# Performance work log

Hardware: AMD Instinct MI355X
Metric: run time of the kernel (lower is better)

The kernel has to match this reference:

```python
import jax, jax.numpy as jnp
import numpy as np

N_NODES = 512
HEADS = 4
CO = 64        # per-head out channels (PyG GATConv out_channels)
NEG_SLOPE = 0.2  # PyG GATConv default negative_slope


def setup_inputs() -> dict:
    key = jax.random.key(0)
    k0, k1, k2, k3, k4 = jax.random.split(key, 5)
    B, C, T, N = 8, 64, 12, N_NODES
    E = 8192
    x = jax.random.normal(k0, (B, C, T, N), dtype=jnp.float32)
    edge_index = jax.random.randint(k1, (2, E), 0, N, dtype=jnp.int32)
    # learned params of GATConv(in=64, out=64, heads=4, concat=False)
    W = jax.random.normal(k2, (C, HEADS * CO), dtype=jnp.float32) / np.sqrt(C).astype(np.float32)
    att_src = jax.random.normal(k3, (HEADS, CO), dtype=jnp.float32) * 0.1
    att_dst = jax.random.normal(k4, (HEADS, CO), dtype=jnp.float32) * 0.1
    bias = jnp.zeros((CO,), dtype=jnp.float32)
    return {"x": x, "edge_index": edge_index, "W": W,
            "att_src": att_src, "att_dst": att_dst, "bias": bias}


def reference(x, edge_index, W, att_src, att_dst, bias):
    # x: [B, C, T, N] -> batch of G = B*T graphs, all sharing edge_index.
    B, C, T, N = x.shape
    H, Co = att_src.shape
    G = B * T
    xg = x.transpose(0, 2, 3, 1).reshape(G, N, C)              # [G,N,C]
    h = (xg @ W).reshape(G, N, H, Co)                          # [G,N,H,Co]
    a_src = jnp.einsum('gnhc,hc->gnh', h, att_src)             # [G,N,H]
    a_dst = jnp.einsum('gnhc,hc->gnh', h, att_dst)             # [G,N,H]
    # add self loops (PyG GATConv default)
    loops = jnp.arange(N, dtype=edge_index.dtype)
    src = jnp.concatenate([edge_index[0], loops])              # [E']
    dst = jnp.concatenate([edge_index[1], loops])              # [E']
    # attention logits per edge, leading edge axis for segment ops
    logits = jax.nn.leaky_relu(a_src[:, src] + a_dst[:, dst], NEG_SLOPE)  # [G,E',H]
    logits = logits.transpose(1, 0, 2)                         # [E',G,H]
    m = jax.ops.segment_max(logits, dst, num_segments=N)       # [N,G,H]
    e = jnp.exp(logits - m[dst])
    s = jax.ops.segment_sum(e, dst, num_segments=N)            # [N,G,H]
    alpha = e / s[dst]                                         # [E',G,H]  (dropout off: eval)
    msg = alpha[..., None] * h[:, src].transpose(1, 0, 2, 3)   # [E',G,H,Co]
    out = jax.ops.segment_sum(msg, dst, num_segments=N)        # [N,G,H,Co]
    out = out.mean(axis=2) + bias                              # [N,G,Co]  concat=False -> head mean
    out = out.transpose(1, 0, 2).reshape(B, T, N, Co)          # [B,T,N,Co]
    return out.transpose(0, 3, 1, 2)                           # [B,Co,T,N]
```

## Files before the change

### kernel.cpp

```cpp
#include <hip/hip_runtime.h>

#define B_  8
#define C_  64
#define T_  12
#define N_  512
#define E_  8192
#define H_  4
#define CO_ 64
#define G_  (B_ * T_)
#define EP_ (E_ + N_)
#define MAXDEG 128
#define POISON 0xAAAAAAAAu

typedef __bf16 bf16x8 __attribute__((ext_vector_type(8)));
typedef unsigned short usx8 __attribute__((ext_vector_type(8)));
typedef float  f32x4  __attribute__((ext_vector_type(4)));

static __device__ __forceinline__ unsigned short f2bf(float f) {
    unsigned int u = __float_as_uint(f);
    return (unsigned short)((u + 0x7fffu + ((u >> 16) & 1u)) >> 16);
}

__global__ __launch_bounds__(256) void k_prep(
    const float* __restrict__ x, const int* __restrict__ ei,
    const float* __restrict__ W,
    const float* __restrict__ att_src, const float* __restrict__ att_dst,
    unsigned short* __restrict__ xtb, float* __restrict__ as_, float* __restrict__ ad_,
    unsigned int* __restrict__ cnt, int* __restrict__ srclist,
    unsigned short* __restrict__ Wfrag)
{
    int bid = blockIdx.x, tid = threadIdx.x;

    if (bid >= 768) {
        if (bid < 800) {
            int e = (bid - 768) * 256 + tid;
            int d = ei[E_ + e], s = ei[e];
            unsigned int pos = atomicAdd(&cnt[d], 1u) - POISON;
            srclist[d * MAXDEG + pos] = s;
        } else {
            int base = (bid - 800) * 2048;
            #pragma unroll
            for (int it = 0; it < 8; ++it) {
                int idx = base + it * 256 + tid;
                int c  = idx >> 8, r = idx & 255;
                int hh = r >> 6,  co = r & 63;
                int k  = hh * 64 + c;
                int ks = k >> 5, kq = (k >> 3) & 3, j = k & 7;
                int nt = co >> 4, l = kq * 16 + (co & 15);
                Wfrag[(size_t)((ks * 4 + nt) * 64 + l) * 8 + j] = f2bf(W[idx]);
            }
        }
        return;
    }

    __shared__ float xs[64][65];
    __shared__ float Wls[64][4], Wld[64][4];
    __shared__ float sa[64][5], sd[64][5];

    int lane = tid & 63, q = tid >> 6;

    {
        float s1 = 0.f, s2 = 0.f;
        const float4* w4 = reinterpret_cast<const float4*>(W + lane * 256 + q * 64);
        const float4* a1 = reinterpret_cast<const float4*>(att_src + q * 64);
        const float4* a2 = reinterpret_cast<const float4*>(att_dst + q * 64);
        #pragma unroll
        for (int j = 0; j < 16; ++j) {
            float4 w = w4[j], u = a1[j], v = a2[j];
            s1 += w.x * u.x + w.y * u.y + w.z * u.z + w.w * u.w;
            s2 += w.x * v.x + w.y * v.y + w.z * v.z + w.w * v.w;
        }
        Wls[lane][q] = s1;
        Wld[lane][q] = s2;
    }

    int g  = bid >> 3, tl = bid & 7;
    int b  = g / T_, t = g - b * T_;
    int n0 = tl * 64;

    #pragma unroll
    for (int i = 0; i < 16; ++i) {
        int c = q + i * 4;
        xs[c][lane] = x[((size_t)(b * C_ + c) * T_ + t) * N_ + n0 + lane];
    }
    __syncthreads();

    float s1 = 0.f, s2 = 0.f;
    for (int c = 0; c < 64; ++c) {
        float v = xs[c][lane];
        s1 += v * Wls[c][q];
        s2 += v * Wld[c][q];
    }
    sa[lane][q] = s1;
    sd[lane][q] = s2;

    #pragma unroll
    for (int i = 0; i < 16; ++i) {
        int nl = q + i * 4;
        xtb[((size_t)(g * N_ + n0 + nl)) * 64 + lane] = f2bf(xs[lane][nl]);
    }
    __syncthreads();

    int nl = tid >> 2, hh = tid & 3;
    as_[((size_t)(g * N_ + n0 + nl)) * 4 + hh] = sa[nl][hh];
    ad_[((size_t)(g * N_ + n0 + nl)) * 4 + hh] = sd[nl][hh];
}

__global__ __launch_bounds__(256) void k_aggr(
    const unsigned short* __restrict__ xtb, const float* __restrict__ as_,
    const float* __restrict__ ad_,
    const unsigned int* __restrict__ cnt, const int* __restrict__ srclist,
    unsigned short* __restrict__ zb)
{
    __shared__ float wbuf[2][MAXDEG][4][4];
    __shared__ int   ssrc[2][MAXDEG];
    int tid  = threadIdx.x;
    int wave = tid >> 6, lane = tid & 63;
    int xcd  = blockIdx.x & 7;
    int slot = blockIdx.x >> 3;
    int np   = slot & 255;
    int gq   = slot >> 8;
    int g0   = xcd * 12 + gq * 4;
    int n0   = np * 2;
    int dg[2] = {(int)(cnt[n0] - POISON), (int)(cnt[n0 + 1] - POISON)};
    int dtot  = max(dg[0], dg[1]) + 1;

    {
        int row = tid >> 7, t2 = tid & 127;
        ssrc[row][t2] = (t2 < dg[row]) ? srclist[(n0 + row) * MAXDEG + t2]
                                       : (n0 + row);
    }

    int sub = tid & 15, p = tid >> 4;
    int hh = sub & 3, gl = sub >> 2;
    int gg = g0 + gl;
    #pragma unroll
    for (int u = 0; u < 2; ++u) {
        float adv = ad_[((size_t)(gg * N_ + n0 + u)) * 4 + hh];
        for (int e = p; e < dg[u]; e += 16) {
            int s = srclist[(n0 + u) * MAXDEG + e];
            float v = as_[((size_t)(gg * N_ + s)) * 4 + hh] + adv;
            v = v > 0.f ? v : 0.2f * v;
            wbuf[u][e][gl][hh] = __expf(v);
        }
        if (p == 0) {
            float v = as_[((size_t)(gg * N_ + n0 + u)) * 4 + hh] + adv;
            v = v > 0.f ? v : 0.2f * v;
            wbuf[u][dg[u]][gl][hh] = __expf(v);
        }
        for (int e = dg[u] + 1 + p; e < dtot; e += 16)
            wbuf[u][e][gl][hh] = 0.f;
    }
    __syncthreads();

    int g   = g0 + wave;
    int u   = lane >> 5;
    int ch2 = (lane & 31) * 2;
    const unsigned short* xg = xtb + ((size_t)g * N_) * 64 + ch2;

    float zA0 = 0.f, zA1 = 0.f, zA2 = 0.f, zA3 = 0.f;
    float zB0 = 0.f, zB1 = 0.f, zB2 = 0.f, zB3 = 0.f;
    float s0 = 0.f, s1 = 0.f, s2 = 0.f, s3 = 0.f;
    int e = 0;
    for (; e + 8 <= dtot; e += 8) {
        unsigned int xv[8];
        #pragma unroll
        for (int j = 0; j < 8; ++j)
            xv[j] = *reinterpret_cast<const unsigned int*>(xg + (size_t)ssrc[u][e + j] * 64);
        #pragma unroll
        for (int j = 0; j < 8; ++j) {
            float x0 = __uint_as_float(xv[j] << 16);
            float x1 = __uint_as_float(xv[j] & 0xffff0000u);
            float4 w = *reinterpret_cast<const float4*>(&wbuf[u][e + j][wave][0]);
            zA0 += w.x * x0;  zB0 += w.x * x1;  s0 += w.x;
            zA1 += w.y * x0;  zB1 += w.y * x1;  s1 += w.y;
            zA2 += w.z * x0;  zB2 += w.z * x1;  s2 += w.z;
            zA3 += w.w * x0;  zB3 += w.w * x1;  s3 += w.w;
        }
    }
    for (; e < dtot; ++e) {
        unsigned int xv = *reinterpret_cast<const unsigned int*>(xg + (size_t)ssrc[u][e] * 64);
        float x0 = __uint_as_float(xv << 16);
        float x1 = __uint_as_float(xv & 0xffff0000u);
        float4 w = *reinterpret_cast<const float4*>(&wbuf[u][e][wave][0]);
        zA0 += w.x * x0;  zB0 += w.x * x1;  s0 += w.x;
        zA1 += w.y * x0;  zB1 += w.y * x1;  s1 += w.y;
        zA2 += w.z * x0;  zB2 += w.z * x1;  s2 += w.z;
        zA3 += w.w * x0;  zB3 += w.w * x1;  s3 += w.w;
    }

    size_t base = ((size_t)g * N_ + n0 + u) * 256 + ch2;
    unsigned int p0 = (unsigned int)f2bf(zA0 / s0) | ((unsigned int)f2bf(zB0 / s0) << 16);
    unsigned int p1 = (unsigned int)f2bf(zA1 / s1) | ((unsigned int)f2bf(zB1 / s1) << 16);
    unsigned int p2 = (unsigned int)f2bf(zA2 / s2) | ((unsigned int)f2bf(zB2 / s2) << 16);
    unsigned int p3 = (unsigned int)f2bf(zA3 / s3) | ((unsigned int)f2bf(zB3 / s3) << 16);
    *reinterpret_cast<unsigned int*>(zb + base +   0) = p0;
    *reinterpret_cast<unsigned int*>(zb + base +  64) = p1;
    *reinterpret_cast<unsigned int*>(zb + base + 128) = p2;
    *reinterpret_cast<unsigned int*>(zb + base + 192) = p3;
}

__global__ __launch_bounds__(256) void k_out(
    const unsigned short* __restrict__ zb, const unsigned short* __restrict__ Wfrag,
    const float* __restrict__ bias, float* __restrict__ out)
{
    __shared__ char lds[32768];
    unsigned short (*Bfr)[4][64][8] = (unsigned short (*)[4][64][8])lds;
    float (*tl)[65] = (float (*)[65])lds;

    int bid  = blockIdx.x;
    int xcd  = bid & 7;
    int r    = bid >> 3;
    int g    = xcd * 12 + (r >> 3);
    int tile = r & 7;
    int b    = g / T_, t = g - b * T_;
    int n0   = tile * 64;
    int tid  = threadIdx.x;

    {
        const float4* src = reinterpret_cast<const float4*>(Wfrag);
        float4* dst = reinterpret_cast<float4*>(&Bfr[0][0][0][0]);
        #pragma unroll
        for (int it = 0; it < 8; ++it)
            dst[tid + it * 256] = src[tid + it * 256];
    }
    __syncthreads();

    int i = tid >> 6, l = tid & 63;
    int m = l & 15, quad = l >> 4;
    const unsigned short* zrow = zb + ((size_t)(g * N_) + n0 + i * 16 + m) * 256 + quad * 8;

    f32x4 acc[4];
    #pragma unroll
    for (int nt = 0; nt < 4; ++nt) acc[nt] = (f32x4){0.f, 0.f, 0.f, 0.f};

    #pragma unroll
    for (int ks = 0; ks < 8; ++ks) {
        usx8 ua = *reinterpret_cast<const usx8*>(zrow + ks * 32);
        bf16x8 a = __builtin_bit_cast(bf16x8, ua);
        #pragma unroll
        for (int nt = 0; nt < 4; ++nt) {
            bf16x8 bw = *reinterpret_cast<bf16x8*>(&Bfr[ks][nt][l][0]);
            acc[nt] = __builtin_amdgcn_mfma_f32_16x16x32_bf16(a, bw, acc[nt], 0, 0, 0);
        }
    }
    __syncthreads();

    #pragma unroll
    for (int nt = 0; nt < 4; ++nt) {
        int co = nt * 16 + m;
        float bv = bias[co];
        #pragma unroll
        for (int rr = 0; rr < 4; ++rr) {
            int row = i * 16 + quad * 4 + rr;
            tl[row][co] = 0.25f * acc[nt][rr] + bv;
        }
    }
    __syncthreads();

    #pragma unroll
    for (int it = 0; it < 16; ++it) {
        int c = i + it * 4;
        out[((size_t)(b * CO_ + c) * T_ + t) * N_ + n0 + l] = tl[l][c];
    }
}

extern "C" void kernel_launch(void* const* d_in, const int* in_sizes, int n_in,
                              void* d_out, int out_size, void* d_ws, size_t ws_size,
                              hipStream_t stream) {
    const float* x       = (const float*)d_in[0];
    const int*   ei      = (const int*)  d_in[1];
    const float* W       = (const float*)d_in[2];
    const float* att_src = (const float*)d_in[3];
    const float* att_dst = (const float*)d_in[4];
    const float* bias    = (const float*)d_in[5];
    float* out = (float*)d_out;

    char* p = (char*)d_ws;
    unsigned short* xtb = (unsigned short*)p; p += (size_t)G_ * N_ * C_ * sizeof(unsigned short);
    unsigned short* zb  = (unsigned short*)p; p += (size_t)G_ * N_ * 256 * sizeof(unsigned short);
    float* as_     = (float*)p;  p += (size_t)G_ * N_ * H_ * sizeof(float);
    float* ad_     = (float*)p;  p += (size_t)G_ * N_ * H_ * sizeof(float);
    unsigned short* Wfrag = (unsigned short*)p; p += 64 * 256 * sizeof(unsigned short);
    unsigned int* cnt = (unsigned int*)p; p += 512 * sizeof(unsigned int);
    int* srclist   = (int*)p;    p += N_ * MAXDEG * sizeof(int);

    k_prep  <<<808,     256, 0, stream>>>(x, ei, W, att_src, att_dst,
                                          xtb, as_, ad_, cnt, srclist, Wfrag);
    k_aggr  <<<8 * 768, 256, 0, stream>>>(xtb, as_, ad_, cnt, srclist, zb);
    k_out   <<<G_ * 8,  256, 0, stream>>>(zb, Wfrag, bias, out);
}
```

Before: 123.9 us.

## Fuse aggregation and output projection into one kernel via swizzled LDS tile

After: 124.8 us. No clear change (+0.8%).

```diff
diff --git a/kernel.cpp b/kernel.cpp
--- a/kernel.cpp
+++ b/kernel.cpp
@@ -60,18 +60,27 @@
     int lane = tid & 63, q = tid >> 6;
 
     {
-        float s1 = 0.f, s2 = 0.f;
-        const float4* w4 = reinterpret_cast<const float4*>(W + lane * 256 + q * 64);
-        const float4* a1 = reinterpret_cast<const float4*>(att_src + q * 64);
-        const float4* a2 = reinterpret_cast<const float4*>(att_dst + q * 64);
+        const float4* W4 = reinterpret_cast<const float4*>(W);
+        const float4* A4 = reinterpret_cast<const float4*>(att_src);
+        const float4* D4 = reinterpret_cast<const float4*>(att_dst);
+        float4 uu = A4[lane];
+        float4 vv = D4[lane];
         #pragma unroll
-        for (int j = 0; j < 16; ++j) {
-            float4 w = w4[j], u = a1[j], v = a2[j];
-            s1 += w.x * u.x + w.y * u.y + w.z * u.z + w.w * u.w;
-            s2 += w.x * v.x + w.y * v.y + w.z * v.z + w.w * v.w;
-        }
-        Wls[lane][q] = s1;
-        Wld[lane][q] = s2;
+        for (int it = 0; it < 16; ++it) {
+            int idx4 = tid + it * 256;
+            float4 w = W4[idx4];
+            float s1 = w.x*uu.x + w.y*uu.y + w.z*uu.z + w.w*uu.w;
+            float s2 = w.x*vv.x + w.y*vv.y + w.z*vv.z + w.w*vv.w;
+            #pragma unroll
+            for (int off = 1; off < 16; off <<= 1) {
+                s1 += __shfl_xor(s1, off, 64);
+                s2 += __shfl_xor(s2, off, 64);
+            }
+            if ((lane & 15) == 0) {
+                Wls[q + it * 4][lane >> 4] = s1;
+                Wld[q + it * 4][lane >> 4] = s2;
+            }
+        }
     }
 
     int g  = bid >> 3, tl = bid & 7;
@@ -106,129 +115,118 @@
     ad_[((size_t)(g * N_ + n0 + nl)) * 4 + hh] = sd[nl][hh];
 }
 
-__global__ __launch_bounds__(256) void k_aggr(
+__global__ __launch_bounds__(256) void k_fused(
     const unsigned short* __restrict__ xtb, const float* __restrict__ as_,
     const float* __restrict__ ad_,
     const unsigned int* __restrict__ cnt, const int* __restrict__ srclist,
-    unsigned short* __restrict__ zb)
+    const unsigned short* __restrict__ Wfrag, const float* __restrict__ bias,
+    float* __restrict__ out)
 {
-    __shared__ float wbuf[2][MAXDEG][4][4];
-    __shared__ int   ssrc[2][MAXDEG];
+    __shared__ __align__(16) char lds[53248];
+    float* wb  = reinterpret_cast<float*>(lds + 32768);
+    int*   ss  = reinterpret_cast<int*>(lds + 49152);
+    float (*tl)[65] = reinterpret_cast<float (*)[65]>(lds + 32768);
+
+    int bid  = blockIdx.x;
+    int xcd  = bid & 7, rest = bid >> 3;
+    int gq   = rest % 12, tile = rest / 12;
+    int g    = xcd * 12 + gq;
+    int n0   = tile * 64;
+    int b    = g / T_, t = g - b * T_;
     int tid  = threadIdx.x;
     int wave = tid >> 6, lane = tid & 63;
-    int xcd  = blockIdx.x & 7;
-    int slot = blockIdx.x >> 3;
-    int np   = slot & 255;
-    int gq   = slot >> 8;
-    int g0   = xcd * 12 + gq * 4;
-    int n0   = np * 2;
-    int dg[2] = {(int)(cnt[n0] - POISON), (int)(cnt[n0 + 1] - POISON)};
-    int dtot  = max(dg[0], dg[1]) + 1;
-
-    {
-        int row = tid >> 7, t2 = tid & 127;
-        ssrc[row][t2] = (t2 < dg[row]) ? srclist[(n0 + row) * MAXDEG + t2]
-                                       : (n0 + row);
-    }
-
-    int sub = tid & 15, p = tid >> 4;
-    int hh = sub & 3, gl = sub >> 2;
-    int gg = g0 + gl;
-    #pragma unroll
-    for (int u = 0; u < 2; ++u) {
-        float adv = ad_[((size_t)(gg * N_ + n0 + u)) * 4 + hh];
-        for (int e = p; e < dg[u]; e += 16) {
-            int s = srclist[(n0 + u) * MAXDEG + e];
-            float v = as_[((size_t)(gg * N_ + s)) * 4 + hh] + adv;
-            v = v > 0.f ? v : 0.2f * v;
-            wbuf[u][e][gl][hh] = __expf(v);
-        }
-        if (p == 0) {
-            float v = as_[((size_t)(gg * N_ + n0 + u)) * 4 + hh] + adv;
-            v = v > 0.f ? v : 0.2f * v;
-            wbuf[u][dg[u]][gl][hh] = __expf(v);
-        }
-        for (int e = dg[u] + 1 + p; e < dtot; e += 16)
-            wbuf[u][e][gl][hh] = 0.f;
-    }
-    __syncthreads();
-
-    int g   = g0 + wave;
-    int u   = lane >> 5;
-    int ch2 = (lane & 31) * 2;
+
+    int u    = lane >> 5;
+    int slot = wave * 2 + u;
+    int ch2  = (lane & 31) * 2;
     const unsigned short* xg = xtb + ((size_t)g * N_) * 64 + ch2;
 
-    float zA0 = 0.f, zA1 = 0.f, zA2 = 0.f, zA3 = 0.f;
-    float zB0 = 0.f, zB1 = 0.f, zB2 = 0.f, zB3 = 0.f;
-    float s0 = 0.f, s1 = 0.f, s2 = 0.f, s3 = 0.f;
-    int e = 0;
-    for (; e + 8 <= dtot; e += 8) {
-        unsigned int xv[8];
-        #pragma unroll
-        for (int j = 0; j < 8; ++j)
-            xv[j] = *reinterpret_cast<const unsigned int*>(xg + (size_t)ssrc[u][e + j] * 64);
-        #pragma unroll
-        for (int j = 0; j < 8; ++j) {
-            float x0 = __uint_as_float(xv[j] << 16);
-            float x1 = __uint_as_float(xv[j] & 0xffff0000u);
-            float4 w = *reinterpret_cast<const float4*>(&wbuf[u][e + j][wave][0]);
+    int fslot = tid >> 5;
+    int fhh   = tid & 3;
+    int fp    = (tid >> 2) & 7;
+    int fe    = tid & 31;
+
+    for (int pass = 0; pass < 8; ++pass) {
+        int nb = n0 + pass * 8;
+
+        {
+            int node = nb + fslot;
+            int dgS  = (int)(cnt[node] - POISON);
+            int dgP  = (int)(cnt[nb + (fslot ^ 1)] - POISON);
+            int dtf  = max(dgS, dgP) + 1;
+            float adv = ad_[((size_t)(g * N_ + node)) * 4 + fhh];
+            for (int e = fp; e < dgS; e += 8) {
+                int s = srclist[node * MAXDEG + e];
+                float v = as_[((size_t)(g * N_ + s)) * 4 + fhh] + adv;
+                v = v > 0.f ? v : 0.2f * v;
+                wb[((fslot * MAXDEG) + e) * 4 + fhh] = __expf(v);
+            }
+            if (fp == 0) {
+                float v = as_[((size_t)(g * N_ + node)) * 4 + fhh] + adv;
+                v = v > 0.f ? v : 0.2f * v;
+                wb[((fslot * MAXDEG) + dgS) * 4 + fhh] = __expf(v);
+            }
+            for (int e = dgS + 1 + fp; e < dtf; e += 8)
+                wb[((fslot * MAXDEG) + e) * 4 + fhh] = 0.f;
+            for (int e = fe; e < dtf; e += 32)
+                ss[fslot * MAXDEG + e] = (e < dgS) ? srclist[node * MAXDEG + e] : node;
+        }
+        __syncthreads();
+
+        int dgA  = (int)(cnt[nb + wave * 2]     - POISON);
+        int dgB  = (int)(cnt[nb + wave * 2 + 1] - POISON);
+        int dtot = max(dgA, dgB) + 1;
+        const int*   sbase = ss + slot * MAXDEG;
+        const float* wbase = wb + slot * MAXDEG * 4;
+
+        float zA0=0.f, zA1=0.f, zA2=0.f, zA3=0.f;
+        float zB0=0.f, zB1=0.f, zB2=0.f, zB3=0.f;
+        float s0=0.f, s1=0.f, s2=0.f, s3=0.f;
+        int e = 0;
+        for (; e + 8 <= dtot; e += 8) {
+            unsigned int xv[8];
+            #pragma unroll
+            for (int j = 0; j < 8; ++j)
+                xv[j] = *reinterpret_cast<const unsigned int*>(xg + (size_t)sbase[e + j] * 64);
+            #pragma unroll
+            for (int j = 0; j < 8; ++j) {
+                float x0 = __uint_as_float(xv[j] << 16);
+                float x1 = __uint_as_float(xv[j] & 0xffff0000u);
+                float4 w = *reinterpret_cast<const float4*>(wbase + (e + j) * 4);
+                zA0 += w.x * x0;  zB0 += w.x * x1;  s0 += w.x;
+                zA1 += w.y * x0;  zB1 += w.y * x1;  s1 += w.y;
+                zA2 += w.z * x0;  zB2 += w.z * x1;  s2 += w.z;
+                zA3 += w.w * x0;  zB3 += w.w * x1;  s3 += w.w;
+            }
+        }
+        for (; e < dtot; ++e) {
+            unsigned int xv = *reinterpret_cast<const unsigned int*>(xg + (size_t)sbase[e] * 64);
+            float x0 = __uint_as_float(xv << 16);
+            float x1 = __uint_as_float(xv & 0xffff0000u);
+            float4 w = *reinterpret_cast<const float4*>(wbase + e * 4);
             zA0 += w.x * x0;  zB0 += w.x * x1;  s0 += w.x;
             zA1 += w.y * x0;  zB1 += w.y * x1;  s1 += w.y;
             zA2 += w.z * x0;  zB2 += w.z * x1;  s2 += w.z;
             zA3 += w.w * x0;  zB3 += w.w * x1;  s3 += w.w;
         }
-    }
-    for (; e < dtot; ++e) {
-        unsigned int xv = *reinterpret_cast<const unsigned int*>(xg + (size_t)ssrc[u][e] * 64);
-        float x0 = __uint_as_float(xv << 16);
-        float x1 = __uint_as_float(xv & 0xffff0000u);
-        float4 w = *reinterpret_cast<const float4*>(&wbuf[u][e][wave][0]);
-        zA0 += w.x * x0;  zB0 += w.x * x1;  s0 += w.x;
-        zA1 += w.y * x0;  zB1 += w.y * x1;  s1 += w.y;
-        zA2 += w.z * x0;  zB2 += w.z * x1;  s2 += w.z;
-        zA3 += w.w * x0;  zB3 += w.w * x1;  s3 += w.w;
-    }
-
-    size_t base = ((size_t)g * N_ + n0 + u) * 256 + ch2;
-    unsigned int p0 = (unsigned int)f2bf(zA0 / s0) | ((unsigned int)f2bf(zB0 / s0) << 16);
-    unsigned int p1 = (unsigned int)f2bf(zA1 / s1) | ((unsigned int)f2bf(zB1 / s1) << 16);
-    unsigned int p2 = (unsigned int)f2bf(zA2 / s2) | ((unsigned int)f2bf(zB2 / s2) << 16);
-    unsigned int p3 = (unsigned int)f2bf(zA3 / s3) | ((unsigned int)f2bf(zB3 / s3) << 16);
-    *reinterpret_cast<unsigned int*>(zb + base +   0) = p0;
-    *reinterpret_cast<unsigned int*>(zb + base +  64) = p1;
-    *reinterpret_cast<unsigned int*>(zb + base + 128) = p2;
-    *reinterpret_cast<unsigned int*>(zb + base + 192) = p3;
-}
-
-__global__ __launch_bounds__(256) void k_out(
-    const unsigned short* __restrict__ zb, const unsigned short* __restrict__ Wfrag,
-    const float* __restrict__ bias, float* __restrict__ out)
-{
-    __shared__ char lds[32768];
-    unsigned short (*Bfr)[4][64][8] = (unsigned short (*)[4][64][8])lds;
-    float (*tl)[65] = (float (*)[65])lds;
-
-    int bid  = blockIdx.x;
-    int xcd  = bid & 7;
-    int r    = bid >> 3;
-    int g    = xcd * 12 + (r >> 3);
-    int tile = r & 7;
-    int b    = g / T_, t = g - b * T_;
-    int n0   = tile * 64;
-    int tid  = threadIdx.x;
-
-    {
-        const float4* src = reinterpret_cast<const float4*>(Wfrag);
-        float4* dst = reinterpret_cast<float4*>(&Bfr[0][0][0][0]);
-        #pragma unroll
-        for (int it = 0; it < 8; ++it)
-            dst[tid + it * 256] = src[tid + it * 256];
-    }
-    __syncthreads();
-
-    int i = tid >> 6, l = tid & 63;
-    int m = l & 15, quad = l >> 4;
-    const unsigned short* zrow = zb + ((size_t)(g * N_) + n0 + i * 16 + m) * 256 + quad * 8;
+
+        int nl = pass * 8 + slot;
+        unsigned int sw  = (unsigned int)((nl & 7) << 4);
+        unsigned int o0  = (unsigned int)(nl * 512 + ch2 * 2);
+        unsigned int p0 = (unsigned int)f2bf(zA0 / s0) | ((unsigned int)f2bf(zB0 / s0) << 16);
+        unsigned int p1 = (unsigned int)f2bf(zA1 / s1) | ((unsigned int)f2bf(zB1 / s1) << 16);
+        unsigned int p2 = (unsigned int)f2bf(zA2 / s2) | ((unsigned int)f2bf(zB2 / s2) << 16);
+        unsigned int p3 = (unsigned int)f2bf(zA3 / s3) | ((unsigned int)f2bf(zB3 / s3) << 16);
+        *reinterpret_cast<unsigned int*>(lds + ((o0 +   0) ^ sw)) = p0;
+        *reinterpret_cast<unsigned int*>(lds + ((o0 + 128) ^ sw)) = p1;
+        *reinterpret_cast<unsigned int*>(lds + ((o0 + 256) ^ sw)) = p2;
+        *reinterpret_cast<unsigned int*>(lds + ((o0 + 384) ^ sw)) = p3;
+        __syncthreads();
+    }
+
+    int m = lane & 15, quad = lane >> 4;
+    int nrow = wave * 16 + m;
+    unsigned int swr = (unsigned int)((m & 7) << 4);
 
     f32x4 acc[4];
     #pragma unroll
@@ -236,15 +234,17 @@
 
     #pragma unroll
     for (int ks = 0; ks < 8; ++ks) {
-        usx8 ua = *reinterpret_cast<const usx8*>(zrow + ks * 32);
-        bf16x8 a = __builtin_bit_cast(bf16x8, ua);
+        unsigned int ro = (unsigned int)(nrow * 512 + quad * 16 + ks * 64);
+        uint4 za = *reinterpret_cast<const uint4*>(lds + (ro ^ swr));
+        bf16x8 a = __builtin_bit_cast(bf16x8, za);
         #pragma unroll
         for (int nt = 0; nt < 4; ++nt) {
-            bf16x8 bw = *reinterpret_cast<bf16x8*>(&Bfr[ks][nt][l][0]);
+            usx8 ub = *reinterpret_cast<const usx8*>(
+                Wfrag + (size_t)(((ks * 4 + nt) * 64 + lane) * 8));
+            bf16x8 bw = __builtin_bit_cast(bf16x8, ub);
             acc[nt] = __builtin_amdgcn_mfma_f32_16x16x32_bf16(a, bw, acc[nt], 0, 0, 0);
         }
     }
-    __syncthreads();
 
     #pragma unroll
     for (int nt = 0; nt < 4; ++nt) {
@@ -252,7 +252,7 @@
         float bv = bias[co];
         #pragma unroll
         for (int rr = 0; rr < 4; ++rr) {
-            int row = i * 16 + quad * 4 + rr;
+            int row = wave * 16 + quad * 4 + rr;
             tl[row][co] = 0.25f * acc[nt][rr] + bv;
         }
     }
@@ -260,8 +260,8 @@
 
     #pragma unroll
     for (int it = 0; it < 16; ++it) {
-        int c = i + it * 4;
-        out[((size_t)(b * CO_ + c) * T_ + t) * N_ + n0 + l] = tl[l][c];
+        int c = wave + it * 4;
+        out[((size_t)(b * CO_ + c) * T_ + t) * N_ + n0 + lane] = tl[lane][c];
     }
 }
 
@@ -278,15 +278,13 @@
 
     char* p = (char*)d_ws;
     unsigned short* xtb = (unsigned short*)p; p += (size_t)G_ * N_ * C_ * sizeof(unsigned short);
-    unsigned short* zb  = (unsigned short*)p; p += (size_t)G_ * N_ * 256 * sizeof(unsigned short);
     float* as_     = (float*)p;  p += (size_t)G_ * N_ * H_ * sizeof(float);
     float* ad_     = (float*)p;  p += (size_t)G_ * N_ * H_ * sizeof(float);
     unsigned short* Wfrag = (unsigned short*)p; p += 64 * 256 * sizeof(unsigned short);
     unsigned int* cnt = (unsigned int*)p; p += 512 * sizeof(unsigned int);
     int* srclist   = (int*)p;    p += N_ * MAXDEG * sizeof(int);
 
-    k_prep  <<<808,     256, 0, stream>>>(x, ei, W, att_src, att_dst,
-                                          xtb, as_, ad_, cnt, srclist, Wfrag);
-    k_aggr  <<<8 * 768, 256, 0, stream>>>(xtb, as_, ad_, cnt, srclist, zb);
-    k_out   <<<G_ * 8,  256, 0, stream>>>(zb, Wfrag, bias, out);
-}
+    k_prep  <<<808, 256, 0, stream>>>(x, ei, W, att_src, att_dst,
+                                      xtb, as_, ad_, cnt, srclist, Wfrag);
+    k_fused <<<768, 256, 0, stream>>>(xtb, as_, ad_, cnt, srclist, Wfrag, bias, out);
+}
```
